# Kernel tuning notes

Hardware: AMD Instinct MI355X
Metric: run time of the kernel (lower is better)

## Reference

```python
import jax, jax.numpy as jnp
import numpy as np

N, E, IN, H, C = 50000, 800000, 128, 128, 4


def setup_inputs() -> dict:
    key = jax.random.key(0)
    ks = jax.random.split(key, 16)
    s = 0.05
    x = jax.random.normal(ks[0], (N, IN), jnp.float32)
    edge_index = jax.random.randint(ks[1], (2, E), 0, N, jnp.int32)
    inp = {"x": x, "edge_index": edge_index}
    dims = [(IN, H), (H, H), (H, H)]  # per-layer (fan_in, fan_out)
    for i, (fi, fo) in enumerate(dims):
        inp[f"Wl{i}"] = jax.random.normal(ks[2 + 3 * i], (fo, fi), jnp.float32) * s  # neighbor lin (lin_l)
        inp[f"bl{i}"] = jax.random.normal(ks[3 + 3 * i], (fo,), jnp.float32) * s
        inp[f"Wr{i}"] = jax.random.normal(ks[4 + 3 * i], (fo, fi), jnp.float32) * s  # root lin (lin_r, no bias)
    inp["Wh1"] = jax.random.normal(ks[11], (H // 2, H), jnp.float32) * s
    inp["bh1"] = jax.random.normal(ks[12], (H // 2,), jnp.float32) * s
    inp["Wh2"] = jax.random.normal(ks[13], (C, H // 2), jnp.float32) * s
    inp["bh2"] = jax.random.normal(ks[14], (C,), jnp.float32) * s
    return inp


def _sage(x, src, dst, Wl, bl, Wr):
    # mean aggregation of source features at destination nodes
    deg = jax.ops.segment_sum(jnp.ones((src.shape[0],), x.dtype), dst, num_segments=N)
    agg = jax.ops.segment_sum(x[src], dst, num_segments=N)
    mean = agg / jnp.maximum(deg, 1.0)[:, None]
    return mean @ Wl.T + bl + x @ Wr.T


def reference(x, edge_index, Wl0, bl0, Wr0, Wl1, bl1, Wr1, Wl2, bl2, Wr2, Wh1, bh1, Wh2, bh2):
    src, dst = edge_index[0], edge_index[1]
    h = jax.nn.relu(_sage(x, src, dst, Wl0, bl0, Wr0))
    h = jax.nn.relu(_sage(h, src, dst, Wl1, bl1, Wr1))
    h = jax.nn.relu(_sage(h, src, dst, Wl2, bl2, Wr2))
    # head MLP (dropout is identity in eval)
    h = jax.nn.relu(h @ Wh1.T + bh1)
    return h @ Wh2.T + bh2
```

## Files before the change

### kernel.cpp

```cpp
#include <hip/hip_runtime.h>
#include <cstdint>
#include <cstddef>


typedef __attribute__((ext_vector_type(8))) short short8;
typedef __attribute__((ext_vector_type(8))) unsigned short ushort8;
typedef __attribute__((ext_vector_type(4))) float floatx4;

#define BSHIFT 7
#define MAXB 512

__device__ __forceinline__ float bf2f(unsigned short h) {
    return __uint_as_float(((unsigned int)h) << 16);
}
__device__ __forceinline__ void split2(float x, unsigned short& hi, unsigned short& lo) {
    unsigned int u = __float_as_uint(x);
    hi = (unsigned short)(u >> 16);
    float r = x - __uint_as_float(u & 0xFFFF0000u);
    lo = (unsigned short)(__float_as_uint(r) >> 16);
}


__global__ __launch_bounds__(256) void prep_kernel(
    const float* __restrict__ x, unsigned short* __restrict__ xH, int total4,
    const float* __restrict__ w0, const float* __restrict__ w1,
    const float* __restrict__ w2, const float* __restrict__ w3,
    const float* __restrict__ w4, const float* __restrict__ w5,
    const float* __restrict__ wh1,
    unsigned short* __restrict__ WH, unsigned short* __restrict__ WL,
    const int* __restrict__ dst, int E, int* __restrict__ bh, int NBUCK,
    int XB, int WB, int HB) {
    __shared__ int lh[MAXB];
    int bid = blockIdx.x;
    int tid = threadIdx.x;
    if (bid < XB) {
        int i = bid * 256 + tid;
        if (i < total4) {
            float4 v = ((const float4*)x)[i];
            ushort4 h;
            h.x = (unsigned short)(__float_as_uint(v.x) >> 16);
            h.y = (unsigned short)(__float_as_uint(v.y) >> 16);
            h.z = (unsigned short)(__float_as_uint(v.z) >> 16);
            h.w = (unsigned short)(__float_as_uint(v.w) >> 16);
            ((ushort4*)xH)[i] = h;
        }
    } else if (bid < XB + WB) {
        int wb = bid - XB;
        if (wb < 96) {
            int m = wb >> 4;
            const float* src = (m == 0) ? w0 : (m == 1) ? w1 : (m == 2) ? w2
                               : (m == 3) ? w3 : (m == 4) ? w4 : w5;
            int i = ((wb & 15) << 8) + tid;
            float4 v = ((const float4*)src)[i];
            unsigned short h0, h1, h2, h3, l0, l1, l2, l3;
            split2(v.x, h0, l0); split2(v.y, h1, l1);
            split2(v.z, h2, l2); split2(v.w, h3, l3);
            ((ushort4*)(WH + (size_t)m * 16384))[i] = make_ushort4(h0, h1, h2, h3);
            ((ushort4*)(WL + (size_t)m * 16384))[i] = make_ushort4(l0, l1, l2, l3);
        } else {
            int i = ((wb - 96) << 8) + tid;
            if (i < 2048) {
                float4 v = ((const float4*)wh1)[i];
                unsigned short h0, h1, h2, h3, l0, l1, l2, l3;
                split2(v.x, h0, l0); split2(v.y, h1, l1);
                split2(v.z, h2, l2); split2(v.w, h3, l3);
                ((ushort4*)(WH + (size_t)6 * 16384))[i] = make_ushort4(h0, h1, h2, h3);
                ((ushort4*)(WL + (size_t)6 * 16384))[i] = make_ushort4(l0, l1, l2, l3);
            }
        }
    } else {
        int hbid = bid - XB - WB;
        for (int i = tid; i < NBUCK; i += 256) lh[i] = 0;
        __syncthreads();
        for (int e = hbid * 256 + tid; e < E; e += HB * 256)
            atomicAdd(&lh[dst[e] >> BSHIFT], 1);
        __syncthreads();
        for (int i = tid; i < NBUCK; i += 256)
            if (lh[i]) atomicAdd(&bh[i], lh[i]);
    }
}


__global__ __launch_bounds__(512) void bucket_scan_kernel(const int* __restrict__ bh,
                                                          int* __restrict__ bucket_base,
                                                          int* __restrict__ bucket_cursor,
                                                          int* __restrict__ row_ptr,
                                                          int NBUCK, int N, int E) {
    __shared__ int s[512];
    int tid = threadIdx.x;
    int v = (tid < NBUCK) ? bh[tid] : 0;
    s[tid] = v;
    __syncthreads();
#pragma unroll
    for (int off = 1; off < 512; off <<= 1) {
        int t = (tid >= off) ? s[tid - off] : 0;
        __syncthreads();
        s[tid] += t;
        __syncthreads();
    }
    int excl = s[tid] - v;
    if (tid < NBUCK) { bucket_base[tid] = excl; bucket_cursor[tid] = excl; }
    if (tid == 0) { bucket_base[NBUCK] = E; row_ptr[N] = E; }
}


__global__ __launch_bounds__(256) void binsort_kernel(const int* __restrict__ src,
                                                      const int* __restrict__ dst,
                                                      int E, int CHUNK,
                                                      int* __restrict__ bucket_cursor,
                                                      unsigned int* __restrict__ ebuf,
                                                      int NBUCK) {
    __shared__ int lh[MAXB];
    __shared__ int lcur[MAXB];
    __shared__ int gbase[MAXB];
    int e0 = blockIdx.x * CHUNK;
    int e1 = e0 + CHUNK; if (e1 > E) e1 = E;
    for (int i = threadIdx.x; i < NBUCK; i += 256) { lh[i] = 0; lcur[i] = 0; }
    __syncthreads();
    for (int e = e0 + threadIdx.x; e < e1; e += 256)
        atomicAdd(&lh[dst[e] >> BSHIFT], 1);
    __syncthreads();
    for (int b = threadIdx.x; b < NBUCK; b += 256) {
        int c = lh[b];
        gbase[b] = c ? atomicAdd(&bucket_cursor[b], c) : 0;
    }
    __syncthreads();
    for (int e = e0 + threadIdx.x; e < e1; e += 256) {
        int d = dst[e];
        int s = src[e];
        int b = d >> BSHIFT;
        int off = atomicAdd(&lcur[b], 1);
        ebuf[gbase[b] + off] = (unsigned int)s | ((unsigned int)d << 16);
    }
}


__global__ __launch_bounds__(256) void bucket_fill_kernel(const int* __restrict__ bucket_base,
                                                          const unsigned int* __restrict__ ebuf,
                                                          int* __restrict__ row_ptr,
                                                          int* __restrict__ col, int N) {
    __shared__ int cnt[256];
    __shared__ int scan[256];
    __shared__ int cur[256];
    int b = blockIdx.x;
    int nbase = b << BSHIFT;
    int tid = threadIdx.x;
    int gB = bucket_base[b];
    int gEnd = bucket_base[b + 1];
    cnt[tid] = 0;
    __syncthreads();
    for (int e = gB + tid; e < gEnd; e += 256)
        atomicAdd(&cnt[(ebuf[e] >> 16) - nbase], 1);
    __syncthreads();
    int v = cnt[tid];
    scan[tid] = v;
    __syncthreads();
#pragma unroll
    for (int off = 1; off < 256; off <<= 1) {
        int t = (tid >= off) ? scan[tid - off] : 0;
        __syncthreads();
        scan[tid] += t;
        __syncthreads();
    }
    int excl = scan[tid] - v;
    int n = nbase + tid;
    if (tid < 128 && n < N) row_ptr[n] = gB + excl;
    cur[tid] = gB + excl;
    __syncthreads();
    for (int e = gB + tid; e < gEnd; e += 256) {
        unsigned int pv = ebuf[e];
        int s = (int)(pv & 0xFFFFu);
        int d = (int)(pv >> 16);
        int p = atomicAdd(&cur[d - nbase], 1);
        col[p] = s;
    }
}


__global__ __launch_bounds__(256) void agg_mean_kernel(
    const unsigned short* __restrict__ inH,
    const int* __restrict__ row_ptr, const int* __restrict__ col,
    unsigned short* __restrict__ mH, int N) {
    int wave = threadIdx.x >> 6;
    int lane = threadIdx.x & 63;
    int n = blockIdx.x * 4 + wave;
    if (n >= N) return;
    int quarter = lane >> 4;
    int li = lane & 15;
    int beg = row_ptr[n];
    int end = row_ptr[n + 1];
    float a0 = 0.f, a1 = 0.f, a2 = 0.f, a3 = 0.f;
    float a4 = 0.f, a5 = 0.f, a6 = 0.f, a7 = 0.f;
    float b0 = 0.f, b1 = 0.f, b2 = 0.f, b3 = 0.f;
    float b4 = 0.f, b5 = 0.f, b6 = 0.f, b7 = 0.f;
    int i = beg + quarter;
    for (; i + 4 < end; i += 8) {
        int s0 = col[i], s1 = col[i + 4];
        ushort8 h0 = ((const ushort8*)(inH + (size_t)s0 * 128))[li];
        ushort8 h1 = ((const ushort8*)(inH + (size_t)s1 * 128))[li];
        a0 += bf2f(h0[0]); a1 += bf2f(h0[1]); a2 += bf2f(h0[2]); a3 += bf2f(h0[3]);
        a4 += bf2f(h0[4]); a5 += bf2f(h0[5]); a6 += bf2f(h0[6]); a7 += bf2f(h0[7]);
        b0 += bf2f(h1[0]); b1 += bf2f(h1[1]); b2 += bf2f(h1[2]); b3 += bf2f(h1[3]);
        b4 += bf2f(h1[4]); b5 += bf2f(h1[5]); b6 += bf2f(h1[6]); b7 += bf2f(h1[7]);
    }
    for (; i < end; i += 4) {
        int s0 = col[i];
        ushort8 h0 = ((const ushort8*)(inH + (size_t)s0 * 128))[li];
        a0 += bf2f(h0[0]); a1 += bf2f(h0[1]); a2 += bf2f(h0[2]); a3 += bf2f(h0[3]);
        a4 += bf2f(h0[4]); a5 += bf2f(h0[5]); a6 += bf2f(h0[6]); a7 += bf2f(h0[7]);
    }
    a0 += b0; a1 += b1; a2 += b2; a3 += b3;
    a4 += b4; a5 += b5; a6 += b6; a7 += b7;
    a0 += __shfl_down(a0, 16); a1 += __shfl_down(a1, 16);
    a2 += __shfl_down(a2, 16); a3 += __shfl_down(a3, 16);
    a4 += __shfl_down(a4, 16); a5 += __shfl_down(a5, 16);
    a6 += __shfl_down(a6, 16); a7 += __shfl_down(a7, 16);
    a0 += __shfl_down(a0, 32); a1 += __shfl_down(a1, 32);
    a2 += __shfl_down(a2, 32); a3 += __shfl_down(a3, 32);
    a4 += __shfl_down(a4, 32); a5 += __shfl_down(a5, 32);
    a6 += __shfl_down(a6, 32); a7 += __shfl_down(a7, 32);
    if (quarter == 0) {
        int d = end - beg;
        float inv = 1.0f / (float)(d > 0 ? d : 1);
        ushort8 o;
        o[0] = (unsigned short)(__float_as_uint(a0 * inv) >> 16);
        o[1] = (unsigned short)(__float_as_uint(a1 * inv) >> 16);
        o[2] = (unsigned short)(__float_as_uint(a2 * inv) >> 16);
        o[3] = (unsigned short)(__float_as_uint(a3 * inv) >> 16);
        o[4] = (unsigned short)(__float_as_uint(a4 * inv) >> 16);
        o[5] = (unsigned short)(__float_as_uint(a5 * inv) >> 16);
        o[6] = (unsigned short)(__float_as_uint(a6 * inv) >> 16);
        o[7] = (unsigned short)(__float_as_uint(a7 * inv) >> 16);
        ((ushort8*)(mH + (size_t)n * 128))[li] = o;
    }
}


__global__ __launch_bounds__(256, 2) void sage_gemm_mfma(
    const unsigned short* __restrict__ a0H, const unsigned short* __restrict__ a1H,
    const unsigned short* __restrict__ wlH, const unsigned short* __restrict__ wlL,
    const unsigned short* __restrict__ wrH, const unsigned short* __restrict__ wrL,
    const float* __restrict__ bias,
    unsigned short* __restrict__ outH, int N) {
    __shared__ unsigned short Ah[128][40];
    __shared__ unsigned short Wh[128][40];
    __shared__ unsigned short Wl[128][40];
    int tid = threadIdx.x;
    int n0 = blockIdx.x * 128;
    int wv = tid >> 6, lane = tid & 63;
    int wm = wv & 1, wn = wv >> 1;
    int r16 = lane & 15, q = lane >> 4, q8 = q * 8;

    floatx4 acc[4][4];
#pragma unroll
    for (int mi = 0; mi < 4; ++mi)
#pragma unroll
        for (int ni = 0; ni < 4; ++ni) {
            floatx4 z = {0.f, 0.f, 0.f, 0.f};
            acc[mi][ni] = z;
        }

    int tc = (tid & 3) * 8;
    int tr = tid >> 2;

    for (int part = 0; part < 2; ++part) {
        const unsigned short* AH = part ? a1H : a0H;
        const unsigned short* WHp = part ? wrH : wlH;
        const unsigned short* WLp = part ? wrL : wlL;
        for (int kk = 0; kk < 128; kk += 32) {
            __syncthreads();
#pragma unroll
            for (int rr = 0; rr < 2; ++rr) {
                int row = tr + 64 * rr;
                int n = n0 + row;
                ushort8 vh = {0, 0, 0, 0, 0, 0, 0, 0};
                if (n < N) vh = *(const ushort8*)&AH[(size_t)n * 128 + kk + tc];
                *(ushort8*)&Ah[row][tc] = vh;
                *(ushort8*)&Wh[row][tc] = *(const ushort8*)&WHp[(size_t)row * 128 + kk + tc];
                *(ushort8*)&Wl[row][tc] = *(const ushort8*)&WLp[(size_t)row * 128 + kk + tc];
            }
            __syncthreads();
            short8 ah[4];
#pragma unroll
            for (int mi = 0; mi < 4; ++mi)
                ah[mi] = *(const short8*)&Ah[64 * wm + 16 * mi + r16][q8];
#pragma unroll
            for (int ni = 0; ni < 4; ++ni) {
                int row = 64 * wn + 16 * ni + r16;
                short8 bh = *(const short8*)&Wh[row][q8];
                short8 bl = *(const short8*)&Wl[row][q8];
#pragma unroll
                for (int mi = 0; mi < 4; ++mi) {
                    acc[mi][ni] = __builtin_amdgcn_mfma_f32_16x16x32_bf16(ah[mi], bh, acc[mi][ni], 0, 0, 0);
                    acc[mi][ni] = __builtin_amdgcn_mfma_f32_16x16x32_bf16(ah[mi], bl, acc[mi][ni], 0, 0, 0);
                }
            }
        }
    }

#pragma unroll
    for (int ni = 0; ni < 4; ++ni) {
        int j = 64 * wn + 16 * ni + r16;
        float b = bias[j];
#pragma unroll
        for (int mi = 0; mi < 4; ++mi) {
            floatx4 v = acc[mi][ni];
#pragma unroll
            for (int p = 0; p < 4; ++p) {
                int node = n0 + 64 * wm + 16 * mi + 4 * q + p;
                if (node < N) {
                    float val = fmaxf(v[p] + b, 0.f);
                    outH[(size_t)node * 128 + j] =
                        (unsigned short)(__float_as_uint(val) >> 16);
                }
            }
        }
    }
}

#define SM_AH 0
#define SM_WH 5120
#define SM_WL 10240
#define SM_HS 0
#define SM_H1 17408

__global__ __launch_bounds__(256, 2) void sage_gemm_head_fused(
    const unsigned short* __restrict__ a0H, const unsigned short* __restrict__ a1H,
    const unsigned short* __restrict__ wlH, const unsigned short* __restrict__ wlL,
    const unsigned short* __restrict__ wrH, const unsigned short* __restrict__ wrL,
    const float* __restrict__ bias,
    const unsigned short* __restrict__ wh1H, const unsigned short* __restrict__ wh1L,
    const float* __restrict__ bh1, const float* __restrict__ Wh2,
    const float* __restrict__ bh2, float* __restrict__ out, int N) {
    __shared__ unsigned short smem[26112];
    int tid = threadIdx.x;
    int n0 = blockIdx.x * 128;
    int wv = tid >> 6, lane = tid & 63;
    int wm = wv & 1, wn = wv >> 1;
    int r16 = lane & 15, q = lane >> 4, q8 = q * 8;

    floatx4 acc[4][4];
#pragma unroll
    for (int mi = 0; mi < 4; ++mi)
#pragma unroll
        for (int ni = 0; ni < 4; ++ni) {
            floatx4 z = {0.f, 0.f, 0.f, 0.f};
            acc[mi][ni] = z;
        }

    int tc = (tid & 3) * 8;
    int tr = tid >> 2;

    for (int part = 0; part < 2; ++part) {
        const unsigned short* AH = part ? a1H : a0H;
        const unsigned short* WHp = part ? wrH : wlH;
        const unsigned short* WLp = part ? wrL : wlL;
        for (int kk = 0; kk < 128; kk += 32) {
            __syncthreads();
#pragma unroll
            for (int rr = 0; rr < 2; ++rr) {
                int row = tr + 64 * rr;
                int n = n0 + row;
                ushort8 vh = {0, 0, 0, 0, 0, 0, 0, 0};
                if (n < N) vh = *(const ushort8*)&AH[(size_t)n * 128 + kk + tc];
                *(ushort8*)&smem[SM_AH + row * 40 + tc] = vh;
                *(ushort8*)&smem[SM_WH + row * 40 + tc] = *(const ushort8*)&WHp[(size_t)row * 128 + kk + tc];
                *(ushort8*)&smem[SM_WL + row * 40 + tc] = *(const ushort8*)&WLp[(size_t)row * 128 + kk + tc];
            }
            __syncthreads();
            short8 ah[4];
#pragma unroll
            for (int mi = 0; mi < 4; ++mi)
                ah[mi] = *(const short8*)&smem[SM_AH + (64 * wm + 16 * mi + r16) * 40 + q8];
#pragma unroll
            for (int ni = 0; ni < 4; ++ni) {
                int row = 64 * wn + 16 * ni + r16;
                short8 bh = *(const short8*)&smem[SM_WH + row * 40 + q8];
                short8 bl = *(const short8*)&smem[SM_WL + row * 40 + q8];
#pragma unroll
                for (int mi = 0; mi < 4; ++mi) {
                    acc[mi][ni] = __builtin_amdgcn_mfma_f32_16x16x32_bf16(ah[mi], bh, acc[mi][ni], 0, 0, 0);
                    acc[mi][ni] = __builtin_amdgcn_mfma_f32_16x16x32_bf16(ah[mi], bl, acc[mi][ni], 0, 0, 0);
                }
            }
        }
    }

    __syncthreads();
#pragma unroll
    for (int ni = 0; ni < 4; ++ni) {
        int j = 64 * wn + 16 * ni + r16;
        float b = bias[j];
#pragma unroll
        for (int mi = 0; mi < 4; ++mi) {
            floatx4 v = acc[mi][ni];
#pragma unroll
            for (int p = 0; p < 4; ++p) {
                int row = 64 * wm + 16 * mi + 4 * q + p;
                float val = fmaxf(v[p] + b, 0.f);
                smem[SM_HS + row * 136 + j] = (unsigned short)(__float_as_uint(val) >> 16);
            }
        }
    }
    __syncthreads();

    floatx4 acc2[2][4];
#pragma unroll
    for (int t = 0; t < 2; ++t)
#pragma unroll
        for (int nt = 0; nt < 4; ++nt) {
            floatx4 z = {0.f, 0.f, 0.f, 0.f};
            acc2[t][nt] = z;
        }
#pragma unroll
    for (int ks = 0; ks < 4; ++ks) {
        short8 at[2];
#pragma unroll
        for (int t = 0; t < 2; ++t)
            at[t] = *(const short8*)&smem[SM_HS + (16 * (2 * wv + t) + r16) * 136 + 32 * ks + q8];
#pragma unroll
        for (int nt = 0; nt < 4; ++nt) {
            int jrow = 16 * nt + r16;
            short8 bh = *(const short8*)&wh1H[jrow * 128 + 32 * ks + q8];
            short8 bl = *(const short8*)&wh1L[jrow * 128 + 32 * ks + q8];
#pragma unroll
            for (int t = 0; t < 2; ++t) {
                acc2[t][nt] = __builtin_amdgcn_mfma_f32_16x16x32_bf16(at[t], bh, acc2[t][nt], 0, 0, 0);
                acc2[t][nt] = __builtin_amdgcn_mfma_f32_16x16x32_bf16(at[t], bl, acc2[t][nt], 0, 0, 0);
            }
        }
    }
#pragma unroll
    for (int nt = 0; nt < 4; ++nt) {
        int c = 16 * nt + r16;
        float b1 = bh1[c];
#pragma unroll
        for (int t = 0; t < 2; ++t) {
            floatx4 v = acc2[t][nt];
#pragma unroll
            for (int p = 0; p < 4; ++p) {
                int row = 16 * (2 * wv + t) + 4 * q + p;
                float val = fmaxf(v[p] + b1, 0.f);
                smem[SM_H1 + row * 68 + c] = (unsigned short)(__float_as_uint(val) >> 16);
            }
        }
    }
    __syncthreads();

    {
        int row = tid >> 1;
        int c0 = (tid & 1) * 2;
        int n = n0 + row;
        if (n < N) {
            const float* w0p = Wh2 + (size_t)c0 * 64;
            const float* w1p = w0p + 64;
            float s0 = bh2[c0], s1 = bh2[c0 + 1];
#pragma unroll 16
            for (int k = 0; k < 64; ++k) {
                float hv = bf2f(smem[SM_H1 + row * 68 + k]);
                s0 += hv * w0p[k];
                s1 += hv * w1p[k];
            }
            out[(size_t)n * 4 + c0] = s0;
            out[(size_t)n * 4 + c0 + 1] = s1;
        }
    }
}


extern "C" void kernel_launch(void* const* d_in, const int* in_sizes, int n_in,
                              void* d_out, int out_size, void* d_ws, size_t ws_size,
                              hipStream_t stream) {
    const float* x   = (const float*)d_in[0];
    const int*   ei  = (const int*)d_in[1];
    const float* Wl0 = (const float*)d_in[2];
    const float* bl0 = (const float*)d_in[3];
    const float* Wr0 = (const float*)d_in[4];
    const float* Wl1 = (const float*)d_in[5];
    const float* bl1 = (const float*)d_in[6];
    const float* Wr1 = (const float*)d_in[7];
    const float* Wl2 = (const float*)d_in[8];
    const float* bl2 = (const float*)d_in[9];
    const float* Wr2 = (const float*)d_in[10];
    const float* Wh1 = (const float*)d_in[11];
    const float* bh1 = (const float*)d_in[12];
    const float* Wh2 = (const float*)d_in[13];
    const float* bh2 = (const float*)d_in[14];
    float* out = (float*)d_out;

    const int N = in_sizes[0] / 128;
    const int E = in_sizes[1] / 2;
    const int* src = ei;
    const int* dst = ei + E;
    const int NBUCK = ((N + 127) >> BSHIFT);

    int* row_ptr       = (int*)d_ws;
    int* bh            = row_ptr + N + 1;
    int* bucket_base   = bh + NBUCK;
    int* bucket_cursor = bucket_base + NBUCK + 1;
    unsigned int* ebuf = (unsigned int*)(bucket_cursor + NBUCK);
    int* col           = (int*)(ebuf + E);
    size_t ioff = (((size_t)(N + 1 + 3 * NBUCK + 1 + 2 * (size_t)E)) * sizeof(int) + 255) & ~(size_t)255;
    unsigned short* u0H = (unsigned short*)((char*)d_ws + ioff);
    unsigned short* mHb = u0H + (size_t)N * 128;
    unsigned short* aH  = mHb + (size_t)N * 128;
    unsigned short* WH  = aH + (size_t)N * 128;
    unsigned short* WL  = WH + 6 * 16384 + 8192;

    const int nb4 = (N + 3) / 4;
    const int gb128 = (N + 127) / 128;
    const int CHUNK = 2048;
    const int nchunk = (E + CHUNK - 1) / CHUNK;
    const int XB = (N * 32 + 255) / 256;
    const int WB = 104;
    const int HB = 256;

    hipMemsetAsync(bh, 0, (size_t)NBUCK * sizeof(int), stream);
    prep_kernel<<<XB + WB + HB, 256, 0, stream>>>(x, u0H, N * 32,
                                                  Wl0, Wr0, Wl1, Wr1, Wl2, Wr2, Wh1,
                                                  WH, WL, dst, E, bh, NBUCK, XB, WB, HB);
    bucket_scan_kernel<<<1, 512, 0, stream>>>(bh, bucket_base, bucket_cursor, row_ptr, NBUCK, N, E);
    binsort_kernel<<<nchunk, 256, 0, stream>>>(src, dst, E, CHUNK, bucket_cursor, ebuf, NBUCK);
    bucket_fill_kernel<<<NBUCK, 256, 0, stream>>>(bucket_base, ebuf, row_ptr, col, N);

    agg_mean_kernel<<<nb4, 256, 0, stream>>>(u0H, row_ptr, col, mHb, N);
    sage_gemm_mfma<<<gb128, 256, 0, stream>>>(mHb, u0H,
                                              WH + 0 * 16384, WL + 0 * 16384,
                                              WH + 1 * 16384, WL + 1 * 16384,
                                              bl0, aH, N);
    agg_mean_kernel<<<nb4, 256, 0, stream>>>(aH, row_ptr, col, mHb, N);
    sage_gemm_mfma<<<gb128, 256, 0, stream>>>(mHb, aH,
                                              WH + 2 * 16384, WL + 2 * 16384,
                                              WH + 3 * 16384, WL + 3 * 16384,
                                              bl1, u0H, N);
    agg_mean_kernel<<<nb4, 256, 0, stream>>>(u0H, row_ptr, col, mHb, N);
    sage_gemm_head_fused<<<gb128, 256, 0, stream>>>(mHb, u0H,
                                                    WH + 4 * 16384, WL + 4 * 16384,
                                                    WH + 5 * 16384, WL + 5 * 16384,
                                                    bl2,
                                                    WH + 6 * 16384, WL + 6 * 16384,
                                                    bh1, Wh2, bh2, out, N);
}
```

Measured before the change: 293.0 us.

## Drop histogram memset, unroll aggregation gather, widen GEMM K-tile

The bucket histogram now writes a per-block partial histogram (64 blocks) that the scan kernel sums, so the memset launch and the global atomics go away. The mean-aggregation loop is unrolled to four independent neighbor gathers per iteration to raise memory-level parallelism. The SAGE GEMM stages a 64-wide K slice per LDS load instead of 32, which halves the number of sync rounds but raises LDS use and may reduce occupancy.

```diff
diff --git a/kernel.cpp b/kernel.cpp
--- a/kernel.cpp
+++ b/kernel.cpp
@@ -9,6 +9,7 @@
 
 #define BSHIFT 7
 #define MAXB 512
+#define HBLK 64
 
 __device__ __forceinline__ float bf2f(unsigned short h) {
     return __uint_as_float(((unsigned int)h) << 16);
@@ -29,7 +30,7 @@
     const float* __restrict__ wh1,
     unsigned short* __restrict__ WH, unsigned short* __restrict__ WL,
     const int* __restrict__ dst, int E, int* __restrict__ bh, int NBUCK,
-    int XB, int WB, int HB) {
+    int XB, int WB) {
     __shared__ int lh[MAXB];
     int bid = blockIdx.x;
     int tid = threadIdx.x;
@@ -72,11 +73,11 @@
         int hbid = bid - XB - WB;
         for (int i = tid; i < NBUCK; i += 256) lh[i] = 0;
         __syncthreads();
-        for (int e = hbid * 256 + tid; e < E; e += HB * 256)
+        for (int e = hbid * 256 + tid; e < E; e += HBLK * 256)
             atomicAdd(&lh[dst[e] >> BSHIFT], 1);
         __syncthreads();
         for (int i = tid; i < NBUCK; i += 256)
-            if (lh[i]) atomicAdd(&bh[i], lh[i]);
+            bh[hbid * MAXB + i] = lh[i];
     }
 }
 
@@ -88,7 +89,9 @@
                                                           int NBUCK, int N, int E) {
     __shared__ int s[512];
     int tid = threadIdx.x;
-    int v = (tid < NBUCK) ? bh[tid] : 0;
+    int v = 0;
+    if (tid < NBUCK)
+        for (int r = 0; r < HBLK; ++r) v += bh[r * MAXB + tid];
     s[tid] = v;
     __syncthreads();
 #pragma unroll
@@ -194,14 +197,20 @@
     float b0 = 0.f, b1 = 0.f, b2 = 0.f, b3 = 0.f;
     float b4 = 0.f, b5 = 0.f, b6 = 0.f, b7 = 0.f;
     int i = beg + quarter;
-    for (; i + 4 < end; i += 8) {
-        int s0 = col[i], s1 = col[i + 4];
+    for (; i + 12 < end; i += 16) {
+        int s0 = col[i], s1 = col[i + 4], s2 = col[i + 8], s3 = col[i + 12];
         ushort8 h0 = ((const ushort8*)(inH + (size_t)s0 * 128))[li];
         ushort8 h1 = ((const ushort8*)(inH + (size_t)s1 * 128))[li];
+        ushort8 h2 = ((const ushort8*)(inH + (size_t)s2 * 128))[li];
+        ushort8 h3 = ((const ushort8*)(inH + (size_t)s3 * 128))[li];
         a0 += bf2f(h0[0]); a1 += bf2f(h0[1]); a2 += bf2f(h0[2]); a3 += bf2f(h0[3]);
         a4 += bf2f(h0[4]); a5 += bf2f(h0[5]); a6 += bf2f(h0[6]); a7 += bf2f(h0[7]);
         b0 += bf2f(h1[0]); b1 += bf2f(h1[1]); b2 += bf2f(h1[2]); b3 += bf2f(h1[3]);
         b4 += bf2f(h1[4]); b5 += bf2f(h1[5]); b6 += bf2f(h1[6]); b7 += bf2f(h1[7]);
+        a0 += bf2f(h2[0]); a1 += bf2f(h2[1]); a2 += bf2f(h2[2]); a3 += bf2f(h2[3]);
+        a4 += bf2f(h2[4]); a5 += bf2f(h2[5]); a6 += bf2f(h2[6]); a7 += bf2f(h2[7]);
+        b0 += bf2f(h3[0]); b1 += bf2f(h3[1]); b2 += bf2f(h3[2]); b3 += bf2f(h3[3]);
+        b4 += bf2f(h3[4]); b5 += bf2f(h3[5]); b6 += bf2f(h3[6]); b7 += bf2f(h3[7]);
     }
     for (; i < end; i += 4) {
         int s0 = col[i];
@@ -242,9 +251,9 @@
     const unsigned short* __restrict__ wrH, const unsigned short* __restrict__ wrL,
     const float* __restrict__ bias,
     unsigned short* __restrict__ outH, int N) {
-    __shared__ unsigned short Ah[128][40];
-    __shared__ unsigned short Wh[128][40];
-    __shared__ unsigned short Wl[128][40];
+    __shared__ unsigned short Ah[128][72];
+    __shared__ unsigned short Wh[128][72];
+    __shared__ unsigned short Wl[128][72];
     int tid = threadIdx.x;
     int n0 = blockIdx.x * 128;
     int wv = tid >> 6, lane = tid & 63;
@@ -260,18 +269,18 @@
             acc[mi][ni] = z;
         }
 
-    int tc = (tid & 3) * 8;
-    int tr = tid >> 2;
+    int tc = (tid & 7) * 8;
+    int tr = tid >> 3;
 
     for (int part = 0; part < 2; ++part) {
         const unsigned short* AH = part ? a1H : a0H;
         const unsigned short* WHp = part ? wrH : wlH;
         const unsigned short* WLp = part ? wrL : wlL;
-        for (int kk = 0; kk < 128; kk += 32) {
+        for (int kk = 0; kk < 128; kk += 64) {
             __syncthreads();
 #pragma unroll
-            for (int rr = 0; rr < 2; ++rr) {
-                int row = tr + 64 * rr;
+            for (int rr = 0; rr < 4; ++rr) {
+                int row = tr + 32 * rr;
                 int n = n0 + row;
                 ushort8 vh = {0, 0, 0, 0, 0, 0, 0, 0};
                 if (n < N) vh = *(const ushort8*)&AH[(size_t)n * 128 + kk + tc];
@@ -280,19 +289,23 @@
                 *(ushort8*)&Wl[row][tc] = *(const ushort8*)&WLp[(size_t)row * 128 + kk + tc];
             }
             __syncthreads();
-            short8 ah[4];
-#pragma unroll
-            for (int mi = 0; mi < 4; ++mi)
-                ah[mi] = *(const short8*)&Ah[64 * wm + 16 * mi + r16][q8];
-#pragma unroll
-            for (int ni = 0; ni < 4; ++ni) {
-                int row = 64 * wn + 16 * ni + r16;
-                short8 bh = *(const short8*)&Wh[row][q8];
-                short8 bl = *(const short8*)&Wl[row][q8];
-#pragma unroll
-                for (int mi = 0; mi < 4; ++mi) {
-                    acc[mi][ni] = __builtin_amdgcn_mfma_f32_16x16x32_bf16(ah[mi], bh, acc[mi][ni], 0, 0, 0);
-                    acc[mi][ni] = __builtin_amdgcn_mfma_f32_16x16x32_bf16(ah[mi], bl, acc[mi][ni], 0, 0, 0);
+#pragma unroll
+            for (int s = 0; s < 2; ++s) {
+                int ko = 32 * s + q8;
+                short8 ah[4];
+#pragma unroll
+                for (int mi = 0; mi < 4; ++mi)
+                    ah[mi] = *(const short8*)&Ah[64 * wm + 16 * mi + r16][ko];
+#pragma unroll
+                for (int ni = 0; ni < 4; ++ni) {
+                    int row = 64 * wn + 16 * ni + r16;
+                    short8 bh = *(const short8*)&Wh[row][ko];
+                    short8 bl = *(const short8*)&Wl[row][ko];
+#pragma unroll
+                    for (int mi = 0; mi < 4; ++mi) {
+                        acc[mi][ni] = __builtin_amdgcn_mfma_f32_16x16x32_bf16(ah[mi], bh, acc[mi][ni], 0, 0, 0);
+                        acc[mi][ni] = __builtin_amdgcn_mfma_f32_16x16x32_bf16(ah[mi], bl, acc[mi][ni], 0, 0, 0);
+                    }
                 }
             }
         }
@@ -496,11 +509,11 @@
 
     int* row_ptr       = (int*)d_ws;
     int* bh            = row_ptr + N + 1;
-    int* bucket_base   = bh + NBUCK;
+    int* bucket_base   = bh + HBLK * MAXB;
     int* bucket_cursor = bucket_base + NBUCK + 1;
     unsigned int* ebuf = (unsigned int*)(bucket_cursor + NBUCK);
     int* col           = (int*)(ebuf + E);
-    size_t ioff = (((size_t)(N + 1 + 3 * NBUCK + 1 + 2 * (size_t)E)) * sizeof(int) + 255) & ~(size_t)255;
+    size_t ioff = (((size_t)(N + 1 + HBLK * MAXB + 2 * NBUCK + 1 + 2 * (size_t)E)) * sizeof(int) + 255) & ~(size_t)255;
     unsigned short* u0H = (unsigned short*)((char*)d_ws + ioff);
     unsigned short* mHb = u0H + (size_t)N * 128;
     unsigned short* aH  = mHb + (size_t)N * 128;
@@ -513,12 +526,10 @@
     const int nchunk = (E + CHUNK - 1) / CHUNK;
     const int XB = (N * 32 + 255) / 256;
     const int WB = 104;
-    const int HB = 256;
-
-    hipMemsetAsync(bh, 0, (size_t)NBUCK * sizeof(int), stream);
-    prep_kernel<<<XB + WB + HB, 256, 0, stream>>>(x, u0H, N * 32,
-                                                  Wl0, Wr0, Wl1, Wr1, Wl2, Wr2, Wh1,
-                                                  WH, WL, dst, E, bh, NBUCK, XB, WB, HB);
+
+    prep_kernel<<<XB + WB + HBLK, 256, 0, stream>>>(x, u0H, N * 32,
+                                                    Wl0, Wr0, Wl1, Wr1, Wl2, Wr2, Wh1,
+                                                    WH, WL, dst, E, bh, NBUCK, XB, WB);
     bucket_scan_kernel<<<1, 512, 0, stream>>>(bh, bucket_base, bucket_cursor, row_ptr, NBUCK, N, E);
     binsort_kernel<<<nchunk, 256, 0, stream>>>(src, dst, E, CHUNK, bucket_cursor, ebuf, NBUCK);
     bucket_fill_kernel<<<NBUCK, 256, 0, stream>>>(bucket_base, ebuf, row_ptr, col, N);
```

Result: no change. 296.9 us (+1.3%).
